# Optimization experiments

Measured on AMD Instinct MI355X. Metric: run time of the kernel, lower is better.

The kernel has to match this reference:

```python
import jax, jax.numpy as jnp
import numpy as np

N_BINS = 256
TAU = 0.01
EPS = 1e-10


def setup_inputs() -> dict:
    key = jax.random.key(0)
    x = jax.random.uniform(key, (4, 1, 512, 512), dtype=jnp.float32)
    return {"x": x}


def reference(x):
    B, _, H, W = x.shape
    bins = jnp.linspace(0.0, 1.0, N_BINS, dtype=x.dtype)  # (n_bins,)
    xf = x.reshape(B, H * W, 1)                            # (B, HW, 1)
    diff = xf - bins[None, None, :]                        # (B, HW, n_bins)
    weights = jnp.exp(-jnp.square(diff) / (2.0 * TAU ** 2))
    # soft histogram over pixels, normalized per image
    histogram = weights.sum(axis=1)                        # (B, n_bins)
    histogram = histogram / (histogram.sum(axis=1, keepdims=True) + EPS)
    cdf = jnp.cumsum(histogram, axis=1)                    # (B, n_bins)
    cdf_min = cdf[:, 0:1]
    cdf_normalized = (cdf - cdf_min) / (1.0 - cdf_min + EPS)
    # per-pixel soft lookup into the normalized CDF
    weights_norm = weights / (weights.sum(axis=-1, keepdims=True) + EPS)
    equalized_flat = (weights_norm * cdf_normalized[:, None, :]).sum(axis=-1)  # (B, HW)
    return equalized_flat.reshape(B, 1, H, W)
```

## Files before the change

kernel.cpp:

```cpp
#include <hip/hip_runtime.h>
#include <math.h>

#define N_BINS 256
#define TAU 0.01f
#define EPS 1e-10f
#define HW (512*512)
#define Q 4081
#define QSTRIDE 4096
#define MWIN 208
#define WTAB (2*MWIN+1)
#define WPADN 432
#define NP 27
#define CFP_STRIDE 289
#define NPART 64
#define BMAX 4
#define HSTRIDE 16

__device__ __align__(64) unsigned int g_genA = 0u;
__device__ __align__(64) unsigned int g_genB = 0u;
__device__ __align__(16) float g_hist[2][BMAX][N_BINS * HSTRIDE];

__global__ __launch_bounds__(512) void hist_conv_kernel(const float* __restrict__ x) {
    __shared__ float cfp[16 * CFP_STRIDE];
    __shared__ float wtE[WPADN];
    __shared__ unsigned int sgen;
    const int b   = blockIdx.y;
    const int s   = blockIdx.x;
    const int tid = threadIdx.x;
    const int r   = tid & 15;
    const int t   = tid >> 4;

    const float4* xb = (const float4*)(x + (size_t)b * HW + (size_t)s * 4096);
    const float4 p0 = xb[tid];
    const float4 p1 = xb[512 + tid];

    if (tid == 0)
        sgen = __hip_atomic_load(&g_genA, __ATOMIC_RELAXED, __HIP_MEMORY_SCOPE_AGENT);
    for (int i = tid; i < 16 * CFP_STRIDE; i += 512) cfp[i] = 0.f;
    for (int i = tid; i < WPADN; i += 512) {
        const float d = (float)(i - MWIN) * (1.0f / 4080.f);
        wtE[i] = (i < WTAB) ? __expf(-d * d * (1.0f / (2.0f * TAU * TAU))) : 0.f;
    }
    __syncthreads();
    const int par = (int)(sgen & 1u);

    if (s == 0 && tid < N_BINS)
        __hip_atomic_store(&g_hist[par ^ 1][b][tid * HSTRIDE], 0.f,
                           __ATOMIC_RELAXED, __HIP_MEMORY_SCOPE_AGENT);

    {
        const float4 vv[2] = {p0, p1};
#pragma unroll
        for (int i = 0; i < 2; ++i) {
            const float4 v = vv[i];
            int q0 = __float2int_rn(v.x * 4080.f);
            int q1 = __float2int_rn(v.y * 4080.f);
            int q2 = __float2int_rn(v.z * 4080.f);
            int q3 = __float2int_rn(v.w * 4080.f);
            q0 = min(max(q0, 0), Q - 1); q1 = min(max(q1, 0), Q - 1);
            q2 = min(max(q2, 0), Q - 1); q3 = min(max(q3, 0), Q - 1);
            atomicAdd(&cfp[(q0 & 15) * CFP_STRIDE + (q0 >> 4) + 13], 1.f);
            atomicAdd(&cfp[(q1 & 15) * CFP_STRIDE + (q1 >> 4) + 13], 1.f);
            atomicAdd(&cfp[(q2 & 15) * CFP_STRIDE + (q2 >> 4) + 13], 1.f);
            atomicAdd(&cfp[(q3 & 15) * CFP_STRIDE + (q3 >> 4) + 13], 1.f);
        }
    }
    __syncthreads();

    float v0, v1, v2, v3, v4, v5, v6, v7;
    {
        float creg[34];
        const float* cbase = &cfp[r * CFP_STRIDE + 8 * t];
#pragma unroll
        for (int k = 0; k < 34; ++k) creg[k] = cbase[k];
        float acc[8];
#pragma unroll
        for (int uu = 0; uu < 8; ++uu) acc[uu] = 0.f;
#pragma unroll
        for (int p = 0; p < NP; ++p) {
            const float w = wtE[16 * p + r];
#pragma unroll
            for (int uu = 0; uu < 8; ++uu) acc[uu] += w * creg[uu + p];
        }
        v0 = acc[0]; v1 = acc[1]; v2 = acc[2]; v3 = acc[3];
        v4 = acc[4]; v5 = acc[5]; v6 = acc[6]; v7 = acc[7];
    }

    {
        const bool h1 = (r & 1) != 0;
        float s0 = h1 ? v0 : v1, s1 = h1 ? v2 : v3, s2 = h1 ? v4 : v5, s3 = h1 ? v6 : v7;
        const float q0 = __shfl_xor(s0, 1, 64), q1 = __shfl_xor(s1, 1, 64);
        const float q2 = __shfl_xor(s2, 1, 64), q3 = __shfl_xor(s3, 1, 64);
        const float w0 = (h1 ? v1 : v0) + q0;
        const float w1 = (h1 ? v3 : v2) + q1;
        const float w2 = (h1 ? v5 : v4) + q2;
        const float w3 = (h1 ? v7 : v6) + q3;

        const bool h2 = (r & 2) != 0;
        float u0 = h2 ? w0 : w1, u1 = h2 ? w2 : w3;
        const float e0 = __shfl_xor(u0, 2, 64), e1 = __shfl_xor(u1, 2, 64);
        const float x0 = (h2 ? w1 : w0) + e0;
        const float x1 = (h2 ? w3 : w2) + e1;

        const bool h4 = (r & 4) != 0;
        float u2 = h4 ? x0 : x1;
        const float e2 = __shfl_xor(u2, 4, 64);
        const float y = (h4 ? x1 : x0) + e2;

        const float z = y + __shfl_xor(y, 8, 64);

        if (r < 8)
            atomicAdd(&g_hist[par][b][(8 * t + r) * HSTRIDE], z);
    }

    if (b == 0 && s == 0 && tid == 0)
        __hip_atomic_fetch_add(&g_genB, 1u, __ATOMIC_RELAXED, __HIP_MEMORY_SCOPE_AGENT);
}

__global__ __launch_bounds__(512) void lut_equalize_kernel(const float* __restrict__ x,
                                                           float* __restrict__ out) {
    __shared__ float Tl[QSTRIDE];
    __shared__ float wtE[WPADN];
    __shared__ float cdfnp[288];
    __shared__ float onesp[288];
    __shared__ float wsum[4];
    __shared__ float h0s;
    __shared__ unsigned int sgen;
    const int b    = blockIdx.y;
    const int s    = blockIdx.x;
    const int tid  = threadIdx.x;
    const int r    = tid & 15;
    const int t    = tid >> 4;
    const int lane = tid & 63;

    const float4* xb = (const float4*)(x + (size_t)b * HW + (size_t)s * 4096);
    float4 px[2];
    px[0] = xb[tid];
    px[1] = xb[512 + tid];

    if (tid == 0)
        sgen = __hip_atomic_load(&g_genB, __ATOMIC_RELAXED, __HIP_MEMORY_SCOPE_AGENT);
    for (int i = tid; i < 288; i += 512) {
        cdfnp[i] = 0.f;
        onesp[i] = (i >= 13 && i < 269) ? 1.f : 0.f;
    }
    for (int i = tid; i < WPADN; i += 512) {
        const float d = (float)(i - MWIN) * (1.0f / 4080.f);
        wtE[i] = (i < WTAB) ? __expf(-d * d * (1.0f / (2.0f * TAU * TAU))) : 0.f;
    }
    __syncthreads();
    const int par = (int)((sgen - 1u) & 1u);

    float val = 0.f, hv = 0.f;
    if (tid < N_BINS) {
        hv = __hip_atomic_load(&g_hist[par][b][tid * HSTRIDE], __ATOMIC_RELAXED,
                               __HIP_MEMORY_SCOPE_AGENT);
        val = hv;
#pragma unroll
        for (int d = 1; d < 64; d <<= 1) {
            const float n = __shfl_up(val, (unsigned)d, 64);
            if (lane >= d) val += n;
        }
        if (lane == 63) wsum[tid >> 6] = val;
        if (tid == 0) h0s = hv;
    }
    __syncthreads();
    if (tid < N_BINS) {
        float prefix = 0.f, total = 0.f;
#pragma unroll
        for (int w2 = 0; w2 < 4; ++w2) {
            const float ws = wsum[w2];
            if (w2 < (tid >> 6)) prefix += ws;
            total += ws;
        }
        val += prefix;
        const float inv  = 1.0f / (total + EPS);
        const float cdf0 = h0s * inv;
        cdfnp[tid + 13] = (val * inv - cdf0) / (1.0f - cdf0 + EPS);
    }
    __syncthreads();

    {
        float creg[34];
        const int base = 8 * t;
#pragma unroll
        for (int k = 0; k < 34; ++k) creg[k] = cdfnp[base + k];
        float acc[8];
#pragma unroll
        for (int uu = 0; uu < 8; ++uu) acc[uu] = 0.f;

        if (t >= 2 && t <= 29) {
            float swt = 0.f;
#pragma unroll
            for (int p = 0; p < NP; ++p) {
                const float w = wtE[16 * p + r];
                swt += w;
#pragma unroll
                for (int uu = 0; uu < 8; ++uu) acc[uu] += w * creg[uu - p + 26];
            }
            const float dinv = 1.0f / (swt + EPS);
#pragma unroll
            for (int uu = 0; uu < 8; ++uu)
                Tl[16 * (8 * t + uu) + r] = acc[uu] * dinv;
        } else {
            float oreg[34], sw[8];
#pragma unroll
            for (int k = 0; k < 34; ++k) oreg[k] = onesp[base + k];
#pragma unroll
            for (int uu = 0; uu < 8; ++uu) sw[uu] = 0.f;
#pragma unroll
            for (int p = 0; p < NP; ++p) {
                const float w = wtE[16 * p + r];
#pragma unroll
                for (int uu = 0; uu < 8; ++uu) {
                    const int k = uu - p + 26;
                    acc[uu] += w * creg[k];
                    sw[uu]  += w * oreg[k];
                }
            }
#pragma unroll
            for (int uu = 0; uu < 8; ++uu)
                Tl[16 * (8 * t + uu) + r] = acc[uu] / (sw[uu] + EPS);
        }
    }
    __syncthreads();

    float4* ob = (float4*)(out + (size_t)b * HW + (size_t)s * 4096);
#pragma unroll
    for (int i = 0; i < 2; ++i) {
        const float4 v = px[i];
        const float vv[4] = {v.x, v.y, v.z, v.w};
        float res[4];
#pragma unroll
        for (int k2 = 0; k2 < 4; ++k2) {
            const float u = vv[k2] * 4080.f;
            int q = (int)u;
            q = min(max(q, 0), Q - 2);
            const float frac = u - (float)q;
            const float t0 = Tl[q], t1 = Tl[q + 1];
            res[k2] = fmaf(frac, t1 - t0, t0);
        }
        ob[i * 512 + tid] = make_float4(res[0], res[1], res[2], res[3]);
    }

    if (b == 0 && s == 0 && tid == 0)
        __hip_atomic_fetch_add(&g_genA, 1u, __ATOMIC_RELAXED, __HIP_MEMORY_SCOPE_AGENT);
}

extern "C" void kernel_launch(void* const* d_in, const int* in_sizes, int n_in,
                              void* d_out, int out_size, void* d_ws, size_t ws_size,
                              hipStream_t stream) {
    const float* x = (const float*)d_in[0];
    float* out     = (float*)d_out;
    const int B    = in_sizes[0] / HW;

    hist_conv_kernel<<<dim3(NPART, B), 512, 0, stream>>>(x);
    lut_equalize_kernel<<<dim3(NPART, B), 512, 0, stream>>>(x, out);
}
```

Baseline: 70.46 us.

## Replace global atomic histogram with per-block partials reduced in consumer kernel

The histogram kernel now writes each block's 256-bin partial histogram to workspace memory instead of atomically accumulating into a padded global array with generation counters and double buffering. The equalize kernel reads all 64 partials for its image, reduces them in shared memory, and then computes the CDF. This removes contended global atomics and the generation-parity bookkeeping. In exchange every block of the second kernel redundantly reads 64 KB of partials per image.

```diff
diff --git a/kernel.cpp b/kernel.cpp
--- a/kernel.cpp
+++ b/kernel.cpp
@@ -6,24 +6,18 @@
 #define EPS 1e-10f
 #define HW (512*512)
 #define Q 4081
-#define QSTRIDE 4096
 #define MWIN 208
 #define WTAB (2*MWIN+1)
 #define WPADN 432
 #define NP 27
 #define CFP_STRIDE 289
 #define NPART 64
-#define BMAX 4
-#define HSTRIDE 16
-
-__device__ __align__(64) unsigned int g_genA = 0u;
-__device__ __align__(64) unsigned int g_genB = 0u;
-__device__ __align__(16) float g_hist[2][BMAX][N_BINS * HSTRIDE];
-
-__global__ __launch_bounds__(512) void hist_conv_kernel(const float* __restrict__ x) {
+#define REDS 260
+
+__global__ __launch_bounds__(512) void hist_conv_kernel(const float* __restrict__ x,
+                                                        float* __restrict__ partT) {
     __shared__ float cfp[16 * CFP_STRIDE];
     __shared__ float wtE[WPADN];
-    __shared__ unsigned int sgen;
     const int b   = blockIdx.y;
     const int s   = blockIdx.x;
     const int tid = threadIdx.x;
@@ -34,19 +28,12 @@
     const float4 p0 = xb[tid];
     const float4 p1 = xb[512 + tid];
 
-    if (tid == 0)
-        sgen = __hip_atomic_load(&g_genA, __ATOMIC_RELAXED, __HIP_MEMORY_SCOPE_AGENT);
     for (int i = tid; i < 16 * CFP_STRIDE; i += 512) cfp[i] = 0.f;
     for (int i = tid; i < WPADN; i += 512) {
         const float d = (float)(i - MWIN) * (1.0f / 4080.f);
         wtE[i] = (i < WTAB) ? __expf(-d * d * (1.0f / (2.0f * TAU * TAU))) : 0.f;
     }
     __syncthreads();
-    const int par = (int)(sgen & 1u);
-
-    if (s == 0 && tid < N_BINS)
-        __hip_atomic_store(&g_hist[par ^ 1][b][tid * HSTRIDE], 0.f,
-                           __ATOMIC_RELAXED, __HIP_MEMORY_SCOPE_AGENT);
 
     {
         const float4 vv[2] = {p0, p1};
@@ -110,36 +97,28 @@
         const float z = y + __shfl_xor(y, 8, 64);
 
         if (r < 8)
-            atomicAdd(&g_hist[par][b][(8 * t + r) * HSTRIDE], z);
-    }
-
-    if (b == 0 && s == 0 && tid == 0)
-        __hip_atomic_fetch_add(&g_genB, 1u, __ATOMIC_RELAXED, __HIP_MEMORY_SCOPE_AGENT);
+            partT[((size_t)b * NPART + s) * N_BINS + 8 * t + r] = z;
+    }
 }
 
 __global__ __launch_bounds__(512) void lut_equalize_kernel(const float* __restrict__ x,
+                                                           const float* __restrict__ partT,
                                                            float* __restrict__ out) {
-    __shared__ float Tl[QSTRIDE];
+    __shared__ float Tl[16 * N_BINS];
     __shared__ float wtE[WPADN];
     __shared__ float cdfnp[288];
     __shared__ float onesp[288];
+    __shared__ __align__(16) float red[8 * REDS];
     __shared__ float wsum[4];
     __shared__ float h0s;
-    __shared__ unsigned int sgen;
     const int b    = blockIdx.y;
     const int s    = blockIdx.x;
     const int tid  = threadIdx.x;
     const int r    = tid & 15;
     const int t    = tid >> 4;
+    const int wv   = tid >> 6;
     const int lane = tid & 63;
 
-    const float4* xb = (const float4*)(x + (size_t)b * HW + (size_t)s * 4096);
-    float4 px[2];
-    px[0] = xb[tid];
-    px[1] = xb[512 + tid];
-
-    if (tid == 0)
-        sgen = __hip_atomic_load(&g_genB, __ATOMIC_RELAXED, __HIP_MEMORY_SCOPE_AGENT);
     for (int i = tid; i < 288; i += 512) {
         cdfnp[i] = 0.f;
         onesp[i] = (i >= 13 && i < 269) ? 1.f : 0.f;
@@ -148,13 +127,28 @@
         const float d = (float)(i - MWIN) * (1.0f / 4080.f);
         wtE[i] = (i < WTAB) ? __expf(-d * d * (1.0f / (2.0f * TAU * TAU))) : 0.f;
     }
-    __syncthreads();
-    const int par = (int)((sgen - 1u) & 1u);
+
+    const float4* xb = (const float4*)(x + (size_t)b * HW + (size_t)s * 4096);
+    float4 px[2];
+#pragma unroll
+    for (int i = 0; i < 2; ++i) px[i] = xb[i * 512 + tid];
+
+    {
+        const float4* base4 = (const float4*)(partT + (size_t)b * NPART * N_BINS);
+        float4 a4 = make_float4(0.f, 0.f, 0.f, 0.f);
+#pragma unroll
+        for (int rr = 0; rr < 8; ++rr) {
+            const float4 v = base4[(size_t)(8 * wv + rr) * 64 + lane];
+            a4.x += v.x; a4.y += v.y; a4.z += v.z; a4.w += v.w;
+        }
+        ((float4*)&red[wv * REDS])[lane] = a4;
+    }
+    __syncthreads();
 
     float val = 0.f, hv = 0.f;
     if (tid < N_BINS) {
-        hv = __hip_atomic_load(&g_hist[par][b][tid * HSTRIDE], __ATOMIC_RELAXED,
-                               __HIP_MEMORY_SCOPE_AGENT);
+#pragma unroll
+        for (int w2 = 0; w2 < 8; ++w2) hv += red[w2 * REDS + tid];
         val = hv;
 #pragma unroll
         for (int d = 1; d < 64; d <<= 1) {
@@ -242,9 +236,6 @@
         }
         ob[i * 512 + tid] = make_float4(res[0], res[1], res[2], res[3]);
     }
-
-    if (b == 0 && s == 0 && tid == 0)
-        __hip_atomic_fetch_add(&g_genA, 1u, __ATOMIC_RELAXED, __HIP_MEMORY_SCOPE_AGENT);
 }
 
 extern "C" void kernel_launch(void* const* d_in, const int* in_sizes, int n_in,
@@ -254,6 +245,8 @@
     float* out     = (float*)d_out;
     const int B    = in_sizes[0] / HW;
 
-    hist_conv_kernel<<<dim3(NPART, B), 512, 0, stream>>>(x);
-    lut_equalize_kernel<<<dim3(NPART, B), 512, 0, stream>>>(x, out);
+    float* partT = (float*)d_ws;
+
+    hist_conv_kernel<<<dim3(NPART, B), 512, 0, stream>>>(x, partT);
+    lut_equalize_kernel<<<dim3(NPART, B), 512, 0, stream>>>(x, partT, out);
 }
```

Result: faster. 67.00 us (-4.9%).
